# Kernel tuning notes

Measured on AMD Instinct MI355X. Metric: run time of the kernel, lower is better.

The kernel has to match this reference:

```python
import jax, jax.numpy as jnp
import numpy as np

B = 262144
IN, H = 2, 50


def setup_inputs() -> dict:
    key = jax.random.key(0)
    ks = jax.random.split(key, 12)
    k = 1.0 / np.sqrt(H)
    u = lambda kk, shape: jax.random.uniform(kk, shape, jnp.float32, -k, k)
    return {
        "s": jax.random.normal(ks[0], (B, IN), jnp.float32),
        "h": jax.random.normal(ks[1], (B, H), jnp.float32),
        "w_ih": u(ks[2], (3 * H, IN)),
        "w_hh": u(ks[3], (3 * H, H)),
        "b_ih": u(ks[4], (3 * H,)),
        "b_hh": u(ks[5], (3 * H,)),
        "actor_w": u(ks[6], (2, H)),
        "actor_b": u(ks[7], (2,)),
        "critic_w": u(ks[8], (1, H)),
        "critic_b": u(ks[9], (1,)),
    }


def reference(s, h, w_ih, w_hh, b_ih, b_hh, actor_w, actor_b, critic_w, critic_b):
    # PyTorch GRUCell gate math (gate order: reset, update, new)
    gi = s @ w_ih.T + b_ih          # [B, 3H]
    gh = h @ w_hh.T + b_hh          # [B, 3H]
    i_r, i_z, i_n = jnp.split(gi, 3, axis=1)
    h_r, h_z, h_n = jnp.split(gh, 3, axis=1)
    r = jax.nn.sigmoid(i_r + h_r)
    z = jax.nn.sigmoid(i_z + h_z)
    n = jnp.tanh(i_n + r * h_n)
    h_new = (1.0 - z) * n + z * h   # [B, H]
    c = h_new @ critic_w.T + critic_b            # [B, 1]
    pi = jax.nn.softmax(h_new @ actor_w.T + actor_b, axis=1)  # [B, 2]
    return h_new, c, pi
```

## Files before the change

### kernel.cpp

```cpp
#include <hip/hip_runtime.h>
#include <hip/hip_bf16.h>


#define BDIM 256

typedef __bf16 bf16x8 __attribute__((ext_vector_type(8)));
typedef float f32x4 __attribute__((ext_vector_type(4)));
typedef unsigned __attribute__((may_alias)) u32a;
typedef unsigned short __attribute__((may_alias)) u16a;

__device__ __forceinline__ float bf2f(unsigned short u) {
    union { unsigned u; float f; } x; x.u = ((unsigned)u) << 16; return x.f;
}
__device__ __forceinline__ unsigned short f2bf(float f) {
    union { float f; unsigned u; } x; x.f = f;
    unsigned r = x.u + 0x7fffu + ((x.u >> 16) & 1u);
    return (unsigned short)(r >> 16);
}
__device__ __forceinline__ unsigned packbf(float a, float b) {
    union { __hip_bfloat162 h; unsigned u; } c;
    c.h = __float22bfloat162_rn(make_float2(a, b));
    return c.u;
}
__device__ __forceinline__ bf16x8 ldsfrag(const unsigned short* p) {
    bf16x8 v; __builtin_memcpy(&v, p, 16); return v;
}

template <int CTRL>
__device__ __forceinline__ float dpp_add(float v) {
    int s = __builtin_bit_cast(int, v);
    int r = __builtin_amdgcn_update_dpp(s, s, CTRL, 0xf, 0xf, false);
    return v + __builtin_bit_cast(float, r);
}
__device__ __forceinline__ float row16_sum(float v) {
    v = dpp_add<0x128>(v);
    v = dpp_add<0x124>(v);
    v = dpp_add<0x122>(v);
    v = dpp_add<0x121>(v);
    return v;
}

__global__ __launch_bounds__(BDIM, 2) void gru_fused(
    const float* __restrict__ s,
    const float* __restrict__ h,
    const float* __restrict__ w_ih,
    const float* __restrict__ w_hh,
    const float* __restrict__ b_ih,
    const float* __restrict__ b_hh,
    const float* __restrict__ actor_w,
    const float* __restrict__ actor_b,
    const float* __restrict__ critic_w,
    const float* __restrict__ critic_b,
    float* __restrict__ out,
    int Btot, int nTiles)
{
    __shared__ __align__(16) unsigned short xlds[64 * 72];
    __shared__ __align__(16) unsigned short wlds[1536 * 8];

    const int tid  = threadIdx.x;
    const int wave = tid >> 6;
    const int lane = tid & 63;
    const int c16  = lane & 15;
    const int quad = lane >> 4;
    const int R    = wave * 16;

    u32a* xlds32 = (u32a*)xlds;

    for (int i = tid; i < 2304; i += BDIM)
        xlds32[i] = ((i % 36) == 26) ? 0x00003f80u : 0u;

    for (int e = tid; e < 1536; e += BDIM) {
        int ln = e & 63;
        int ks = (e >> 6) & 1;
        int t  = (e >> 7) & 3;
        int g  = e >> 9;
        int n  = t * 16 + (ln & 15);
        int kbase = ks * 32 + (ln >> 4) * 8;
        unsigned short vals[8];
        if (n < 50) {
            int r = g * 50 + n;
            #pragma unroll
            for (int i = 0; i < 8; ++i) {
                int k = kbase + i;
                float v = 0.f;
                if (k < 50)       v = w_hh[r * 50 + k];
                else if (k == 50) v = (g < 2) ? w_ih[r * 2 + 0] : 0.f;
                else if (k == 51) v = (g < 2) ? w_ih[r * 2 + 1] : 0.f;
                else if (k == 52) {
                    v = b_hh[r];
                    if (g < 2) v += b_ih[r];
                }
                vals[i] = f2bf(v);
            }
        } else {
            #pragma unroll
            for (int i = 0; i < 8; ++i) vals[i] = 0;
        }
        #pragma unroll
        for (int i = 0; i < 8; ++i) wlds[e * 8 + i] = vals[i];
    }

    float wi0[4], wi1[4], bi[4], aw0[4], aw1[4], awc[4];
    #pragma unroll
    for (int t = 0; t < 4; ++t) {
        int j = t * 16 + c16;
        bool ok = (j < 50);
        wi0[t] = ok ? w_ih[(100 + j) * 2 + 0] : 0.f;
        wi1[t] = ok ? w_ih[(100 + j) * 2 + 1] : 0.f;
        bi[t]  = ok ? b_ih[100 + j]           : 0.f;
        aw0[t] = ok ? actor_w[j]              : 0.f;
        aw1[t] = ok ? actor_w[50 + j]         : 0.f;
        awc[t] = ok ? critic_w[j]             : 0.f;
    }
    const float ab0 = actor_b[0], ab1 = actor_b[1], cb = critic_b[0];

    __syncthreads();

    bf16x8 bf[3][4][2];
    #pragma unroll
    for (int g = 0; g < 3; ++g)
        #pragma unroll
        for (int t = 0; t < 4; ++t)
            #pragma unroll
            for (int ks = 0; ks < 2; ++ks)
                bf[g][t][ks] =
                    ldsfrag(&wlds[((g << 9) | (t << 7) | (ks << 6) | lane) * 8]);

    const float2* h2 = (const float2*)h;
    const float2* s2 = (const float2*)s;
    float* oc = out + (long long)Btot * 50;
    float2* opi = (float2*)(out + (long long)Btot * 51);

    float2 pf[7];
    int bt = blockIdx.x;
    {
        long long hb = (long long)(bt * 64 + R) * 25;
        #pragma unroll
        for (int j = 0; j < 6; ++j) pf[j] = h2[hb + lane + j * 64];
        if (lane < 16)      pf[6] = h2[hb + 384 + lane];
        else if (lane < 32) pf[6] = s2[bt * 64 + R + lane - 16];
    }

    while (bt < nTiles) {
        const int rowbase = bt * 64;

        #pragma unroll
        for (int j = 0; j < 6; ++j) {
            int d = lane + j * 64;
            int r = d / 25, dk = d - r * 25;
            xlds32[(R + r) * 36 + dk] = packbf(pf[j].x, pf[j].y);
        }
        if (lane < 16)
            xlds32[(R + 15) * 36 + 9 + lane] = packbf(pf[6].x, pf[6].y);
        else if (lane < 32)
            xlds32[(R + lane - 16) * 36 + 25] = packbf(pf[6].x, pf[6].y);

        asm volatile("" ::: "memory");

        const int nbt = bt + gridDim.x;
        {
            int pb = (nbt < nTiles) ? nbt : bt;
            long long hb = (long long)(pb * 64 + R) * 25;
            #pragma unroll
            for (int j = 0; j < 6; ++j) pf[j] = h2[hb + lane + j * 64];
            if (lane < 16)      pf[6] = h2[hb + 384 + lane];
            else if (lane < 32) pf[6] = s2[pb * 64 + R + lane - 16];
        }

        float2 srow[4];
        #pragma unroll
        for (int reg = 0; reg < 4; ++reg)
            srow[reg] = s2[rowbase + R + quad * 4 + reg];

        const unsigned short* arow = &xlds[(R + c16) * 72 + quad * 8];
        bf16x8 a0 = ldsfrag(arow);
        bf16x8 a1 = ldsfrag(arow + 32);

        float* ob = out + (long long)rowbase * 50;

        float hn_r[4][4];
        #pragma unroll
        for (int t = 0; t < 4; ++t) {
            f32x4 ar = {0.f,0.f,0.f,0.f}, az = ar, an = ar;
            ar = __builtin_amdgcn_mfma_f32_16x16x32_bf16(a0, bf[0][t][0], ar, 0, 0, 0);
            ar = __builtin_amdgcn_mfma_f32_16x16x32_bf16(a1, bf[0][t][1], ar, 0, 0, 0);
            az = __builtin_amdgcn_mfma_f32_16x16x32_bf16(a0, bf[1][t][0], az, 0, 0, 0);
            az = __builtin_amdgcn_mfma_f32_16x16x32_bf16(a1, bf[1][t][1], az, 0, 0, 0);
            an = __builtin_amdgcn_mfma_f32_16x16x32_bf16(a0, bf[2][t][0], an, 0, 0, 0);
            an = __builtin_amdgcn_mfma_f32_16x16x32_bf16(a1, bf[2][t][1], an, 0, 0, 0);

            int j = t * 16 + c16;
            #pragma unroll
            for (int reg = 0; reg < 4; ++reg) {
                int lr = R + quad * 4 + reg;
                float inn = fmaf(srow[reg].y, wi1[t],
                            fmaf(srow[reg].x, wi0[t], bi[t]));
                float rg = __builtin_amdgcn_rcpf(1.f + __expf(-ar[reg]));
                float zg = __builtin_amdgcn_rcpf(1.f + __expf(-az[reg]));
                float x = inn + rg * an[reg];
                float e2 = __expf(2.f * x);
                float ng = 1.f - 2.f * __builtin_amdgcn_rcpf(e2 + 1.f);
                float hv = bf2f(((const u16a*)xlds)[lr * 72 + j]);
                float hnew = fmaf(zg, hv - ng, ng);
                hn_r[reg][t] = (j < 50) ? hnew : 0.f;
                if (j < 50) ob[lr * 50 + j] = hnew;
            }
        }

        float sum0[4], sum1[4], sumc[4];
        #pragma unroll
        for (int reg = 0; reg < 4; ++reg) {
            float p0 = 0.f, p1 = 0.f, pc = 0.f;
            #pragma unroll
            for (int t = 0; t < 4; ++t) {
                p0 = fmaf(hn_r[reg][t], aw0[t], p0);
                p1 = fmaf(hn_r[reg][t], aw1[t], p1);
                pc = fmaf(hn_r[reg][t], awc[t], pc);
            }
            sum0[reg] = row16_sum(p0);
            sum1[reg] = row16_sum(p1);
            sumc[reg] = row16_sum(pc);
        }
        if (c16 < 4) {
            float A0 = (c16 == 0) ? sum0[0] : (c16 == 1) ? sum0[1]
                     : (c16 == 2) ? sum0[2] : sum0[3];
            float A1 = (c16 == 0) ? sum1[0] : (c16 == 1) ? sum1[1]
                     : (c16 == 2) ? sum1[2] : sum1[3];
            float C  = (c16 == 0) ? sumc[0] : (c16 == 1) ? sumc[1]
                     : (c16 == 2) ? sumc[2] : sumc[3];
            int gr = rowbase + R + quad * 4 + c16;
            oc[gr] = C + cb;
            A0 += ab0; A1 += ab1;
            float m = fmaxf(A0, A1);
            float e0 = __expf(A0 - m), e1 = __expf(A1 - m);
            float inv = 1.f / (e0 + e1);
            float2 pv; pv.x = e0 * inv; pv.y = e1 * inv;
            opi[gr] = pv;
        }
        bt = nbt;
    }
}

extern "C" void kernel_launch(void* const* d_in, const int* in_sizes, int n_in,
                              void* d_out, int out_size, void* d_ws, size_t ws_size,
                              hipStream_t stream) {
    const float* s        = (const float*)d_in[0];
    const float* h        = (const float*)d_in[1];
    const float* w_ih     = (const float*)d_in[2];
    const float* w_hh     = (const float*)d_in[3];
    const float* b_ih     = (const float*)d_in[4];
    const float* b_hh     = (const float*)d_in[5];
    const float* actor_w  = (const float*)d_in[6];
    const float* actor_b  = (const float*)d_in[7];
    const float* critic_w = (const float*)d_in[8];
    const float* critic_b = (const float*)d_in[9];
    float* out = (float*)d_out;

    int Btot = in_sizes[1] / 50;
    int nTiles = Btot / 64;
    int grid = nTiles < 1024 ? nTiles : 1024;

    gru_fused<<<grid, BDIM, 0, stream>>>(s, h, w_ih, w_hh, b_ih, b_hh,
                                         actor_w, actor_b, critic_w, critic_b,
                                         out, Btot, nTiles);
}
```

Measured before the change: 146.5 us.

## Load MFMA operands directly from global memory, dropping LDS staging and prefetch

Removes the shared-memory staging of both the weight fragments and the per-tile h/s activations. Each lane now loads its MFMA A and B fragments straight from global memory and packs them to bf16 in registers. The h value used in the gate blend is re-read from global in fp32 rather than taken from the bf16 LDS copy. This drops the LDS writes, the block-wide barrier and the software prefetch of the next tile, but h is now read twice with less coalesced float2 and scalar accesses and no overlap of loads with compute.

Result: slower. 154.0 us (+5.1%).

```diff
diff --git a/kernel.cpp b/kernel.cpp
--- a/kernel.cpp
+++ b/kernel.cpp
@@ -6,24 +6,17 @@
 
 typedef __bf16 bf16x8 __attribute__((ext_vector_type(8)));
 typedef float f32x4 __attribute__((ext_vector_type(4)));
-typedef unsigned __attribute__((may_alias)) u32a;
-typedef unsigned short __attribute__((may_alias)) u16a;
-
-__device__ __forceinline__ float bf2f(unsigned short u) {
-    union { unsigned u; float f; } x; x.u = ((unsigned)u) << 16; return x.f;
-}
-__device__ __forceinline__ unsigned short f2bf(float f) {
-    union { float f; unsigned u; } x; x.f = f;
-    unsigned r = x.u + 0x7fffu + ((x.u >> 16) & 1u);
-    return (unsigned short)(r >> 16);
-}
+
 __device__ __forceinline__ unsigned packbf(float a, float b) {
     union { __hip_bfloat162 h; unsigned u; } c;
     c.h = __float22bfloat162_rn(make_float2(a, b));
     return c.u;
 }
-__device__ __forceinline__ bf16x8 ldsfrag(const unsigned short* p) {
-    bf16x8 v; __builtin_memcpy(&v, p, 16); return v;
+__device__ __forceinline__ bf16x8 pack8(float2 a, float2 b, float2 c, float2 d) {
+    union { unsigned u[4]; bf16x8 v; } r;
+    r.u[0] = packbf(a.x, a.y); r.u[1] = packbf(b.x, b.y);
+    r.u[2] = packbf(c.x, c.y); r.u[3] = packbf(d.x, d.y);
+    return r.v;
 }
 
 template <int CTRL>
@@ -54,9 +47,6 @@
     float* __restrict__ out,
     int Btot, int nTiles)
 {
-    __shared__ __align__(16) unsigned short xlds[64 * 72];
-    __shared__ __align__(16) unsigned short wlds[1536 * 8];
-
     const int tid  = threadIdx.x;
     const int wave = tid >> 6;
     const int lane = tid & 63;
@@ -64,40 +54,43 @@
     const int quad = lane >> 4;
     const int R    = wave * 16;
 
-    u32a* xlds32 = (u32a*)xlds;
-
-    for (int i = tid; i < 2304; i += BDIM)
-        xlds32[i] = ((i % 36) == 26) ? 0x00003f80u : 0u;
-
-    for (int e = tid; e < 1536; e += BDIM) {
-        int ln = e & 63;
-        int ks = (e >> 6) & 1;
-        int t  = (e >> 7) & 3;
-        int g  = e >> 9;
-        int n  = t * 16 + (ln & 15);
-        int kbase = ks * 32 + (ln >> 4) * 8;
-        unsigned short vals[8];
-        if (n < 50) {
+    const float2* s2 = (const float2*)s;
+    const float2 z2 = make_float2(0.f, 0.f);
+
+    bf16x8 wf[3][4][2];
+    #pragma unroll
+    for (int g = 0; g < 3; ++g) {
+        #pragma unroll
+        for (int t = 0; t < 4; ++t) {
+            int n = t * 16 + c16;
+            bool okn = (n < 50);
             int r = g * 50 + n;
-            #pragma unroll
-            for (int i = 0; i < 8; ++i) {
-                int k = kbase + i;
-                float v = 0.f;
-                if (k < 50)       v = w_hh[r * 50 + k];
-                else if (k == 50) v = (g < 2) ? w_ih[r * 2 + 0] : 0.f;
-                else if (k == 51) v = (g < 2) ? w_ih[r * 2 + 1] : 0.f;
-                else if (k == 52) {
-                    v = b_hh[r];
-                    if (g < 2) v += b_ih[r];
+            const float* wr = w_hh + r * 50;
+            float2 q0 = okn ? *(const float2*)(wr + quad * 8 + 0) : z2;
+            float2 q1 = okn ? *(const float2*)(wr + quad * 8 + 2) : z2;
+            float2 q2 = okn ? *(const float2*)(wr + quad * 8 + 4) : z2;
+            float2 q3 = okn ? *(const float2*)(wr + quad * 8 + 6) : z2;
+            wf[g][t][0] = pack8(q0, q1, q2, q3);
+
+            float2 p0 = z2, p1 = z2, p2 = z2, p3 = z2;
+            if (okn) {
+                if (quad < 2) {
+                    int kb = 32 + quad * 8;
+                    p0 = *(const float2*)(wr + kb + 0);
+                    p1 = *(const float2*)(wr + kb + 2);
+                    p2 = *(const float2*)(wr + kb + 4);
+                    p3 = *(const float2*)(wr + kb + 6);
+                } else if (quad == 2) {
+                    p0 = *(const float2*)(wr + 48);
+                    float wx0 = (g < 2) ? w_ih[r * 2 + 0] : 0.f;
+                    float wx1 = (g < 2) ? w_ih[r * 2 + 1] : 0.f;
+                    p1 = make_float2(wx0, wx1);
+                    float bb = b_hh[r] + ((g < 2) ? b_ih[r] : 0.f);
+                    p2 = make_float2(bb, 0.f);
                 }
-                vals[i] = f2bf(v);
-            }
-        } else {
-            #pragma unroll
-            for (int i = 0; i < 8; ++i) vals[i] = 0;
-        }
-        #pragma unroll
-        for (int i = 0; i < 8; ++i) wlds[e * 8 + i] = vals[i];
+            }
+            wf[g][t][1] = pack8(p0, p1, p2, p3);
+        }
     }
 
     float wi0[4], wi1[4], bi[4], aw0[4], aw1[4], awc[4];
@@ -114,67 +107,46 @@
     }
     const float ab0 = actor_b[0], ab1 = actor_b[1], cb = critic_b[0];
 
-    __syncthreads();
-
-    bf16x8 bf[3][4][2];
-    #pragma unroll
-    for (int g = 0; g < 3; ++g)
-        #pragma unroll
-        for (int t = 0; t < 4; ++t)
-            #pragma unroll
-            for (int ks = 0; ks < 2; ++ks)
-                bf[g][t][ks] =
-                    ldsfrag(&wlds[((g << 9) | (t << 7) | (ks << 6) | lane) * 8]);
-
-    const float2* h2 = (const float2*)h;
-    const float2* s2 = (const float2*)s;
     float* oc = out + (long long)Btot * 50;
     float2* opi = (float2*)(out + (long long)Btot * 51);
 
-    float2 pf[7];
     int bt = blockIdx.x;
-    {
-        long long hb = (long long)(bt * 64 + R) * 25;
-        #pragma unroll
-        for (int j = 0; j < 6; ++j) pf[j] = h2[hb + lane + j * 64];
-        if (lane < 16)      pf[6] = h2[hb + 384 + lane];
-        else if (lane < 32) pf[6] = s2[bt * 64 + R + lane - 16];
-    }
-
     while (bt < nTiles) {
         const int rowbase = bt * 64;
 
-        #pragma unroll
-        for (int j = 0; j < 6; ++j) {
-            int d = lane + j * 64;
-            int r = d / 25, dk = d - r * 25;
-            xlds32[(R + r) * 36 + dk] = packbf(pf[j].x, pf[j].y);
-        }
-        if (lane < 16)
-            xlds32[(R + 15) * 36 + 9 + lane] = packbf(pf[6].x, pf[6].y);
-        else if (lane < 32)
-            xlds32[(R + lane - 16) * 36 + 25] = packbf(pf[6].x, pf[6].y);
-
-        asm volatile("" ::: "memory");
-
-        const int nbt = bt + gridDim.x;
-        {
-            int pb = (nbt < nTiles) ? nbt : bt;
-            long long hb = (long long)(pb * 64 + R) * 25;
+        const float* hrow = h + (rowbase + R + c16) * 50;
+        float2 a00 = *(const float2*)(hrow + quad * 8 + 0);
+        float2 a01 = *(const float2*)(hrow + quad * 8 + 2);
+        float2 a02 = *(const float2*)(hrow + quad * 8 + 4);
+        float2 a03 = *(const float2*)(hrow + quad * 8 + 6);
+        float2 b0 = z2, b1 = z2, b2 = z2, b3 = z2;
+        if (quad < 2) {
+            int kb = 32 + quad * 8;
+            b0 = *(const float2*)(hrow + kb + 0);
+            b1 = *(const float2*)(hrow + kb + 2);
+            b2 = *(const float2*)(hrow + kb + 4);
+            b3 = *(const float2*)(hrow + kb + 6);
+        } else if (quad == 2) {
+            b0 = *(const float2*)(hrow + 48);
+            b1 = s2[rowbase + R + c16];
+            b2 = make_float2(1.f, 0.f);
+        }
+
+        float hv[4][4];
+        float2 srow[4];
+        #pragma unroll
+        for (int reg = 0; reg < 4; ++reg) {
+            const float* hr2 = h + (rowbase + R + quad * 4 + reg) * 50;
             #pragma unroll
-            for (int j = 0; j < 6; ++j) pf[j] = h2[hb + lane + j * 64];
-            if (lane < 16)      pf[6] = h2[hb + 384 + lane];
-            else if (lane < 32) pf[6] = s2[pb * 64 + R + lane - 16];
-        }
-
-        float2 srow[4];
-        #pragma unroll
-        for (int reg = 0; reg < 4; ++reg)
+            for (int t = 0; t < 4; ++t) {
+                int j = t * 16 + c16;
+                hv[reg][t] = (j < 50) ? hr2[j] : 0.f;
+            }
             srow[reg] = s2[rowbase + R + quad * 4 + reg];
-
-        const unsigned short* arow = &xlds[(R + c16) * 72 + quad * 8];
-        bf16x8 a0 = ldsfrag(arow);
-        bf16x8 a1 = ldsfrag(arow + 32);
+        }
+
+        bf16x8 a0 = pack8(a00, a01, a02, a03);
+        bf16x8 a1 = pack8(b0, b1, b2, b3);
 
         float* ob = out + (long long)rowbase * 50;
 
@@ -182,12 +154,12 @@
         #pragma unroll
         for (int t = 0; t < 4; ++t) {
             f32x4 ar = {0.f,0.f,0.f,0.f}, az = ar, an = ar;
-            ar = __builtin_amdgcn_mfma_f32_16x16x32_bf16(a0, bf[0][t][0], ar, 0, 0, 0);
-            ar = __builtin_amdgcn_mfma_f32_16x16x32_bf16(a1, bf[0][t][1], ar, 0, 0, 0);
-            az = __builtin_amdgcn_mfma_f32_16x16x32_bf16(a0, bf[1][t][0], az, 0, 0, 0);
-            az = __builtin_amdgcn_mfma_f32_16x16x32_bf16(a1, bf[1][t][1], az, 0, 0, 0);
-            an = __builtin_amdgcn_mfma_f32_16x16x32_bf16(a0, bf[2][t][0], an, 0, 0, 0);
-            an = __builtin_amdgcn_mfma_f32_16x16x32_bf16(a1, bf[2][t][1], an, 0, 0, 0);
+            ar = __builtin_amdgcn_mfma_f32_16x16x32_bf16(a0, wf[0][t][0], ar, 0, 0, 0);
+            ar = __builtin_amdgcn_mfma_f32_16x16x32_bf16(a1, wf[0][t][1], ar, 0, 0, 0);
+            az = __builtin_amdgcn_mfma_f32_16x16x32_bf16(a0, wf[1][t][0], az, 0, 0, 0);
+            az = __builtin_amdgcn_mfma_f32_16x16x32_bf16(a1, wf[1][t][1], az, 0, 0, 0);
+            an = __builtin_amdgcn_mfma_f32_16x16x32_bf16(a0, wf[2][t][0], an, 0, 0, 0);
+            an = __builtin_amdgcn_mfma_f32_16x16x32_bf16(a1, wf[2][t][1], an, 0, 0, 0);
 
             int j = t * 16 + c16;
             #pragma unroll
@@ -200,8 +172,7 @@
                 float x = inn + rg * an[reg];
                 float e2 = __expf(2.f * x);
                 float ng = 1.f - 2.f * __builtin_amdgcn_rcpf(e2 + 1.f);
-                float hv = bf2f(((const u16a*)xlds)[lr * 72 + j]);
-                float hnew = fmaf(zg, hv - ng, ng);
+                float hnew = fmaf(zg, hv[reg][t] - ng, ng);
                 hn_r[reg][t] = (j < 50) ? hnew : 0.f;
                 if (j < 50) ob[lr * 50 + j] = hnew;
             }
@@ -237,7 +208,7 @@
             float2 pv; pv.x = e0 * inv; pv.y = e1 * inv;
             opi[gr] = pv;
         }
-        bt = nbt;
+        bt += gridDim.x;
     }
 }
 
```
